# Kernel optimization log

Hardware: AMD Instinct MI355X
Metric: run time of the kernel (lower is better)

## Reference

```python
import jax, jax.numpy as jnp
import numpy as np

SCALE = 1.0

def setup_inputs() -> dict:
    key = jax.random.key(0)
    ks = jax.random.split(key, 7)
    B, S, I, O, R = 4, 4096, 1024, 1024, 256
    return {
        "x": jax.random.normal(ks[0], (B, S, I), dtype=jnp.float32),
        "base_weight": jax.random.normal(ks[1], (3 * O, I), dtype=jnp.float32) * 0.02,
        "base_bias": jax.random.normal(ks[2], (3 * O,), dtype=jnp.float32) * 0.02,
        "vera_A": jax.random.normal(ks[3], (R, I), dtype=jnp.float32) * 0.02,
        "vera_B": jax.random.normal(ks[4], (O, R), dtype=jnp.float32) * 0.02,
        "vera_d": jax.random.normal(ks[5], (2, R), dtype=jnp.float32) * 0.1,
        "vera_b": jax.random.normal(ks[6], (2, O), dtype=jnp.float32) * 0.1,
    }

def reference(x, base_weight, base_bias, vera_A, vera_B, vera_d, vera_b):
    # delta[k] = scale * diag(vera_b[k]) @ B @ diag(vera_d[k]) @ A  for k in {K, V}
    # implemented as (b[:,None]*B) @ (d[:,None]*A), batched over k via einsum
    O, I = vera_B.shape[0], vera_A.shape[1]
    deltas = SCALE * jnp.einsum("ko,or,kr,ri->koi", vera_b, vera_B, vera_d, vera_A)
    delta = deltas.reshape(2 * O, I)  # (2*O, I) stacked K,V deltas
    # kv_only=True: Q rows get zero delta, then K,V deltas
    zeros = jnp.zeros((base_weight.shape[0] - 2 * O, I), dtype=base_weight.dtype)
    full_delta = jnp.concatenate([zeros, delta], axis=0)  # (3*O, I)
    weight = base_weight + full_delta
    # linear: x @ weight.T + bias -> (B, S, 3*O)
    return jnp.einsum("bsi,oi->bso", x, weight) + base_bias
```

## Files before the change

kernel.cpp:

```cpp
#include <hip/hip_runtime.h>
#include <hip/hip_bf16.h>
#include <cstdint>
#include <cstddef>

typedef __bf16 bf16_t;
typedef __bf16 bf16x8 __attribute__((ext_vector_type(8)));
typedef __bf16 bf16x4 __attribute__((ext_vector_type(4)));
typedef float  f32x4  __attribute__((ext_vector_type(4)));
typedef float  f32x16 __attribute__((ext_vector_type(16)));

#define M_DIM 16384
#define N_DIM 3072
#define K_DIM 1024
#define R_DIM 256
#define O_DIM 1024

#define BM 256
#define BN 256
#define BK 64
#define NTILE (N_DIM / BN)
#define GRID_GEMM ((M_DIM / BM) * NTILE)
#define CHUNK_XCD (GRID_GEMM / 8)
#define SMEM_BYTES 131072

#define REGN(c, isB, kh) ((c) * 32768 + (isB) * 16384 + (kh) * 8192)

__device__ __forceinline__ void gload_lds16(const bf16_t* g, bf16_t* l) {
  __builtin_amdgcn_global_load_lds(
      (__attribute__((address_space(1))) void*)(g),
      (__attribute__((address_space(3))) void*)(l), 16, 0, 0);
}

__global__ __launch_bounds__(256) void prep_all(
    const float* __restrict__ x,
    const float* __restrict__ base_w,
    const float* __restrict__ vA,
    const float* __restrict__ vB,
    const float* __restrict__ vd,
    const float* __restrict__ vb,
    bf16_t* __restrict__ Wf,
    bf16_t* __restrict__ xh)
{
  const int blk = blockIdx.x;
  const int t = threadIdx.x;

  if (blk >= 384) {
    const size_t base = ((size_t)(blk - 384) * 256 + t) * 8;
    const f32x4 v0 = *(const f32x4*)(x + base);
    const f32x4 v1 = *(const f32x4*)(x + base + 4);
    bf16x8 o;
    o[0] = (bf16_t)v0[0]; o[1] = (bf16_t)v0[1]; o[2] = (bf16_t)v0[2]; o[3] = (bf16_t)v0[3];
    o[4] = (bf16_t)v1[0]; o[5] = (bf16_t)v1[1]; o[6] = (bf16_t)v1[2]; o[7] = (bf16_t)v1[3];
    *(bf16x8*)(xh + base) = o;
    return;
  }

  if (blk < 128) {
    const float* src = base_w + (size_t)blk * 8 * K_DIM;
    bf16_t*      dst = Wf + (size_t)blk * 8 * K_DIM;
#pragma unroll
    for (int rr = 0; rr < 8; ++rr) {
      const f32x4 v = *(const f32x4*)(src + rr * K_DIM + t * 4);
      bf16x4 ov;
      ov[0] = (bf16_t)v[0]; ov[1] = (bf16_t)v[1];
      ov[2] = (bf16_t)v[2]; ov[3] = (bf16_t)v[3];
      *(bf16x4*)(dst + rr * K_DIM + t * 4) = ov;
    }
    return;
  }

  const int rb = (blk - 128) * 8;
  const int k  = rb >> 10;
  const int ob = rb & 1023;

  __shared__ float coeffT[R_DIM][8];
  {
    const int r = t;
    const float d = vd[k * R_DIM + r];
#pragma unroll
    for (int rr = 0; rr < 8; ++rr) {
      const int o = ob + rr;
      coeffT[r][rr] = vb[k * O_DIM + o] * vB[(size_t)o * R_DIM + r] * d;
    }
  }
  __syncthreads();

  float acc[8][4];
#pragma unroll
  for (int rr = 0; rr < 8; ++rr)
#pragma unroll
    for (int c = 0; c < 4; ++c) acc[rr][c] = 0.0f;

  for (int r = 0; r < R_DIM; ++r) {
    const f32x4 av = *(const f32x4*)(vA + (size_t)r * K_DIM + t * 4);
    const f32x4 c0 = *(const f32x4*)&coeffT[r][0];
    const f32x4 c1 = *(const f32x4*)&coeffT[r][4];
#pragma unroll
    for (int rr = 0; rr < 8; ++rr) {
      const float cc = (rr < 4) ? c0[rr] : c1[rr - 4];
      acc[rr][0] += cc * av[0];
      acc[rr][1] += cc * av[1];
      acc[rr][2] += cc * av[2];
      acc[rr][3] += cc * av[3];
    }
  }

#pragma unroll
  for (int rr = 0; rr < 8; ++rr) {
    const size_t row = (size_t)(1024 + rb + rr);
    const f32x4 bw = *(const f32x4*)(base_w + row * K_DIM + t * 4);
    bf16x4 ov;
    ov[0] = (bf16_t)(bw[0] + acc[rr][0]);
    ov[1] = (bf16_t)(bw[1] + acc[rr][1]);
    ov[2] = (bf16_t)(bw[2] + acc[rr][2]);
    ov[3] = (bf16_t)(bw[3] + acc[rr][3]);
    *(bf16x4*)(Wf + row * K_DIM + t * 4) = ov;
  }
}

__global__ __launch_bounds__(512, 2) void gemm_qkv(
    const bf16_t* __restrict__ Xh,
    const bf16_t* __restrict__ W,
    const float*  __restrict__ bias,
    float* __restrict__ out)
{
  extern __shared__ __align__(16) bf16_t sm[];

  const int rawbid = blockIdx.x;
  const int bid = (rawbid & 7) * CHUNK_XCD + (rawbid >> 3);
  const int mt = bid / NTILE, nt = bid % NTILE;
  const int m0 = mt * BM, n0 = nt * BN;

  const int t = threadIdx.x;
  const int lane = t & 63;
  const int w = t >> 6;
  const int wm = w >> 2;
  const int wn = w & 3;

  const int srow = t >> 2;
  const int sig  = (t & 3) ^ ((t >> 3) & 3);
  const bf16_t* pA0 = Xh + (size_t)(m0 + srow) * K_DIM + sig * 8;
  const bf16_t* pA1 = pA0 + (size_t)128 * K_DIM;
  const bf16_t* pB0 = W  + (size_t)(n0 + srow) * K_DIM + sig * 8;
  const bf16_t* pB1 = pB0 + (size_t)128 * K_DIM;

  const int l31 = lane & 31;
  const int hi  = lane >> 5;
  const int swz = (l31 >> 1) & 3;
  const int sA  = (wm * 128 + l31) * 32;
  const int sB  = (wn * 64  + l31) * 32;
  const int sl0 = ((0 + hi) ^ swz) * 8;
  const int sl1 = ((2 + hi) ^ swz) * 8;

  f32x16 acc[4][2];
#pragma unroll
  for (int i = 0; i < 4; ++i)
#pragma unroll
    for (int j = 0; j < 2; ++j) acc[i][j] = (f32x16)0.0f;

#define STAGE(isB, c, kh, kb)                                              \
  do {                                                                     \
    const bf16_t* g0 = ((isB) ? pB0 : pA0) + (kb) + (kh) * 32;             \
    const bf16_t* g1 = ((isB) ? pB1 : pA1) + (kb) + (kh) * 32;             \
    bf16_t* l = sm + REGN(c, isB, kh) + w * 512;                           \
    gload_lds16(g0, l);                                                    \
    gload_lds16(g1, l + 4096);                                             \
  } while (0)

#define LOADA4(c, kh, ks)                                                  \
  {                                                                        \
    const bf16_t* base_ = sm + REGN(c, 0, kh) + sA + ((ks) ? sl1 : sl0);   \
    _Pragma("unroll") for (int i = 0; i < 4; ++i)                          \
        a[i] = *(const bf16x8*)(base_ + i * 1024);                         \
  }

#define LOADB2(c, kh, ks)                                                  \
  {                                                                        \
    const bf16_t* base_ = sm + REGN(c, 1, kh) + sB + ((ks) ? sl1 : sl0);   \
    b[0] = *(const bf16x8*)(base_);                                        \
    b[1] = *(const bf16x8*)(base_ + 1024);                                 \
  }

#define MFMA8()                                                            \
  __builtin_amdgcn_s_setprio(1);                                           \
  _Pragma("unroll") for (int i = 0; i < 4; ++i)                            \
    _Pragma("unroll") for (int j = 0; j < 2; ++j)                          \
      acc[i][j] = __builtin_amdgcn_mfma_f32_32x32x16_bf16(                 \
          a[i], b[j], acc[i][j], 0, 0, 0);                                 \
  __builtin_amdgcn_s_setprio(0);

#define WAITV(n) asm volatile("s_waitcnt vmcnt(" #n ")" ::: "memory")
#define BARRIER()                                                          \
  __builtin_amdgcn_s_barrier();                                            \
  asm volatile("" ::: "memory")

  bf16x8 a[4], b[2];

  STAGE(0, 0, 0, 0);
  STAGE(1, 0, 0, 0);
  STAGE(0, 0, 1, 0);
  STAGE(1, 0, 1, 0);
  WAITV(4);
  BARRIER();

  for (int tt = 0; tt < 15; ++tt) {
    const int c = tt & 1, cn = c ^ 1;
    const int kb = (tt + 1) * BK;

    LOADA4(c, 0, 0);
    LOADB2(c, 0, 0);
    STAGE(0, cn, 0, kb);
    BARRIER();
    MFMA8();

    LOADA4(c, 0, 1);
    LOADB2(c, 0, 1);
    STAGE(1, cn, 0, kb);
    WAITV(4);
    BARRIER();
    MFMA8();

    LOADA4(c, 1, 0);
    LOADB2(c, 1, 0);
    STAGE(0, cn, 1, kb);
    BARRIER();
    MFMA8();

    LOADA4(c, 1, 1);
    LOADB2(c, 1, 1);
    STAGE(1, cn, 1, kb);
    WAITV(4);
    BARRIER();
    MFMA8();
  }

  LOADA4(1, 0, 0);
  LOADB2(1, 0, 0);
  BARRIER();
  MFMA8();

  LOADA4(1, 0, 1);
  LOADB2(1, 0, 1);
  WAITV(0);
  BARRIER();
  MFMA8();

  LOADA4(1, 1, 0);
  LOADB2(1, 1, 0);
  BARRIER();
  MFMA8();

  LOADA4(1, 1, 1);
  LOADB2(1, 1, 1);
  BARRIER();
  MFMA8();

  const int hi4 = hi * 4;
#pragma unroll
  for (int j = 0; j < 2; ++j) {
    const int n = n0 + wn * 64 + j * 32 + l31;
    const float bv = bias[n];
#pragma unroll
    for (int i = 0; i < 4; ++i) {
      const size_t mb = (size_t)(m0 + wm * 128 + i * 32 + hi4);
#pragma unroll
      for (int r = 0; r < 16; ++r) {
        const size_t row = mb + (r & 3) + 8 * (r >> 2);
        out[row * N_DIM + n] = acc[i][j][r] + bv;
      }
    }
  }
#undef STAGE
#undef LOADA4
#undef LOADB2
#undef MFMA8
#undef WAITV
#undef BARRIER
}

#define FBM 128
#define FBN 128
#define FBK 32
template <bool PRECONV>
__global__ __launch_bounds__(256) void gemm128(
    const bf16_t* __restrict__ Xh,
    const float*  __restrict__ Xf,
    const bf16_t* __restrict__ W,
    const float*  __restrict__ bias,
    float* __restrict__ out)
{
  __shared__ bf16_t As[FBM * FBK];
  __shared__ bf16_t Bs[FBN * FBK];

  const int rawbid = blockIdx.x;
  const int nblk = (M_DIM / FBM) * (N_DIM / FBN);
  const int bid = (rawbid & 7) * (nblk / 8) + (rawbid >> 3);
  const int nt = bid % (N_DIM / FBN);
  const int mt = bid / (N_DIM / FBN);
  const int m0 = mt * FBM;
  const int n0 = nt * FBN;

  const int t = threadIdx.x;
  const int lane = t & 63;
  const int w = t >> 6;
  const int wm = w >> 1;
  const int wn = w & 1;

  const int r0 = t >> 2;
  const int c0 = (t & 3) * 8;

  const bf16_t* gB0 = W + (size_t)(n0 + r0) * K_DIM + c0;
  const bf16_t* gB1 = gB0 + (size_t)64 * K_DIM;
  bf16_t* lA0 = As + r0 * FBK + c0;
  bf16_t* lA1 = As + (r0 + 64) * FBK + c0;
  bf16_t* lB0 = Bs + r0 * FBK + c0;
  bf16_t* lB1 = Bs + (r0 + 64) * FBK + c0;

  const bf16_t* gA0h = nullptr; const bf16_t* gA1h = nullptr;
  const float*  gA0f = nullptr; const float*  gA1f = nullptr;
  if constexpr (PRECONV) {
    gA0h = Xh + (size_t)(m0 + r0) * K_DIM + c0;
    gA1h = gA0h + (size_t)64 * K_DIM;
  } else {
    gA0f = Xf + (size_t)(m0 + r0) * K_DIM + c0;
    gA1f = gA0f + (size_t)64 * K_DIM;
  }

  f32x4 acc[4][4];
#pragma unroll
  for (int i = 0; i < 4; ++i)
#pragma unroll
    for (int j = 0; j < 4; ++j) acc[i][j] = (f32x4){0.f, 0.f, 0.f, 0.f};

  const int row_a = wm * 64 + (lane & 15);
  const int row_b = wn * 64 + (lane & 15);
  const int kb = (lane >> 4) * 8;

  for (int k0 = 0; k0 < K_DIM; k0 += FBK) {
    if constexpr (PRECONV) {
      gload_lds16(gA0h + k0, lA0);
      gload_lds16(gA1h + k0, lA1);
    } else {
      const f32x4 u0 = *(const f32x4*)(gA0f + k0);
      const f32x4 u1 = *(const f32x4*)(gA0f + k0 + 4);
      const f32x4 u2 = *(const f32x4*)(gA1f + k0);
      const f32x4 u3 = *(const f32x4*)(gA1f + k0 + 4);
      bf16x8 a0, a1;
#pragma unroll
      for (int c = 0; c < 4; ++c) {
        a0[c] = (bf16_t)u0[c]; a0[c + 4] = (bf16_t)u1[c];
        a1[c] = (bf16_t)u2[c]; a1[c + 4] = (bf16_t)u3[c];
      }
      *(bf16x8*)lA0 = a0;
      *(bf16x8*)lA1 = a1;
    }
    gload_lds16(gB0 + k0, lB0);
    gload_lds16(gB1 + k0, lB1);
    __syncthreads();

    bf16x8 a[4], b[4];
#pragma unroll
    for (int i = 0; i < 4; ++i)
      a[i] = *(const bf16x8*)(As + (row_a + i * 16) * FBK + kb);
#pragma unroll
    for (int j = 0; j < 4; ++j)
      b[j] = *(const bf16x8*)(Bs + (row_b + j * 16) * FBK + kb);

#pragma unroll
    for (int i = 0; i < 4; ++i)
#pragma unroll
      for (int j = 0; j < 4; ++j)
        acc[i][j] = __builtin_amdgcn_mfma_f32_16x16x32_bf16(a[i], b[j], acc[i][j], 0, 0, 0);

    __syncthreads();
  }

  const int colg = lane & 15;
  const int rq = (lane >> 4) * 4;
#pragma unroll
  for (int j = 0; j < 4; ++j) {
    const int n = n0 + wn * 64 + j * 16 + colg;
    const float bv = bias[n];
#pragma unroll
    for (int i = 0; i < 4; ++i) {
      const size_t mb = (size_t)(m0 + wm * 64 + i * 16 + rq);
#pragma unroll
      for (int r = 0; r < 4; ++r)
        out[(mb + r) * N_DIM + n] = acc[i][j][r] + bv;
    }
  }
}

extern "C" void kernel_launch(void* const* d_in, const int* in_sizes, int n_in,
                              void* d_out, int out_size, void* d_ws, size_t ws_size,
                              hipStream_t stream) {
  const float* x      = (const float*)d_in[0];
  const float* base_w = (const float*)d_in[1];
  const float* base_b = (const float*)d_in[2];
  const float* vA     = (const float*)d_in[3];
  const float* vB     = (const float*)d_in[4];
  const float* vd     = (const float*)d_in[5];
  const float* vb     = (const float*)d_in[6];
  float* out = (float*)d_out;

  const size_t xh_off   = 8u * 1024 * 1024;
  const size_t xh_bytes = (size_t)M_DIM * K_DIM * sizeof(bf16_t);

  bf16_t* Wf = (bf16_t*)d_ws;
  const bool preconv = ws_size >= xh_off + xh_bytes;
  bf16_t* Xh = preconv ? (bf16_t*)((char*)d_ws + xh_off) : nullptr;

  static int smem_ok = -1;
  if (smem_ok < 0) {
    hipError_t e = hipFuncSetAttribute(
        reinterpret_cast<const void*>(&gemm_qkv),
        hipFuncAttributeMaxDynamicSharedMemorySize, SMEM_BYTES);
    smem_ok = (e == hipSuccess) ? 1 : 0;
  }

  prep_all<<<preconv ? 8576 : 384, 256, 0, stream>>>(x, base_w, vA, vB, vd, vb, Wf, Xh);

  if (preconv && smem_ok == 1) {
    gemm_qkv<<<GRID_GEMM, 512, SMEM_BYTES, stream>>>(Xh, Wf, base_b, out);
  } else if (preconv) {
    gemm128<true><<<(M_DIM / FBM) * (N_DIM / FBN), 256, 0, stream>>>(
        Xh, nullptr, Wf, base_b, out);
  } else {
    gemm128<false><<<(M_DIM / FBM) * (N_DIM / FBN), 256, 0, stream>>>(
        nullptr, x, Wf, base_b, out);
  }
}
```

Baseline: 389.5 us.

## Fuse fp32-to-bf16 conversion of x into the GEMM A-tile loading

Removes the separate pass that converted x to bf16 in workspace, and instead has the main GEMM load fp32 x into registers, convert, and write bf16 to LDS. The A loads are issued one stage ahead and written after a vmcnt wait, while B stays on direct global-to-LDS loads. This eliminates a full read/write pass over the activation, at the cost of doubled A-side global reads across N tiles, extra registers, and extra LDS-wait synchronisation in the main loop.

```diff
diff --git a/kernel.cpp b/kernel.cpp
--- a/kernel.cpp
+++ b/kernel.cpp
@@ -31,29 +31,16 @@
       (__attribute__((address_space(3))) void*)(l), 16, 0, 0);
 }
 
-__global__ __launch_bounds__(256) void prep_all(
-    const float* __restrict__ x,
+__global__ __launch_bounds__(256) void prep_weight(
     const float* __restrict__ base_w,
     const float* __restrict__ vA,
     const float* __restrict__ vB,
     const float* __restrict__ vd,
     const float* __restrict__ vb,
-    bf16_t* __restrict__ Wf,
-    bf16_t* __restrict__ xh)
+    bf16_t* __restrict__ Wf)
 {
   const int blk = blockIdx.x;
   const int t = threadIdx.x;
-
-  if (blk >= 384) {
-    const size_t base = ((size_t)(blk - 384) * 256 + t) * 8;
-    const f32x4 v0 = *(const f32x4*)(x + base);
-    const f32x4 v1 = *(const f32x4*)(x + base + 4);
-    bf16x8 o;
-    o[0] = (bf16_t)v0[0]; o[1] = (bf16_t)v0[1]; o[2] = (bf16_t)v0[2]; o[3] = (bf16_t)v0[3];
-    o[4] = (bf16_t)v1[0]; o[5] = (bf16_t)v1[1]; o[6] = (bf16_t)v1[2]; o[7] = (bf16_t)v1[3];
-    *(bf16x8*)(xh + base) = o;
-    return;
-  }
 
   if (blk < 128) {
     const float* src = base_w + (size_t)blk * 8 * K_DIM;
@@ -119,7 +106,7 @@
 }
 
 __global__ __launch_bounds__(512, 2) void gemm_qkv(
-    const bf16_t* __restrict__ Xh,
+    const float*  __restrict__ X,
     const bf16_t* __restrict__ W,
     const float*  __restrict__ bias,
     float* __restrict__ out)
@@ -139,9 +126,8 @@
 
   const int srow = t >> 2;
   const int sig  = (t & 3) ^ ((t >> 3) & 3);
-  const bf16_t* pA0 = Xh + (size_t)(m0 + srow) * K_DIM + sig * 8;
-  const bf16_t* pA1 = pA0 + (size_t)128 * K_DIM;
-  const bf16_t* pB0 = W  + (size_t)(n0 + srow) * K_DIM + sig * 8;
+  const float*  pX0 = X + (size_t)(m0 + srow) * K_DIM + sig * 8;
+  const bf16_t* pB0 = W + (size_t)(n0 + srow) * K_DIM + sig * 8;
   const bf16_t* pB1 = pB0 + (size_t)128 * K_DIM;
 
   const int l31 = lane & 31;
@@ -158,14 +144,37 @@
 #pragma unroll
     for (int j = 0; j < 2; ++j) acc[i][j] = (f32x16)0.0f;
 
-#define STAGE(isB, c, kh, kb)                                              \
+  f32x4 af[4];
+
+#define BSTAGE(c, kh, kb)                                                  \
   do {                                                                     \
-    const bf16_t* g0 = ((isB) ? pB0 : pA0) + (kb) + (kh) * 32;             \
-    const bf16_t* g1 = ((isB) ? pB1 : pA1) + (kb) + (kh) * 32;             \
-    bf16_t* l = sm + REGN(c, isB, kh) + w * 512;                           \
+    const bf16_t* g0 = pB0 + (kb) + (kh) * 32;                             \
+    const bf16_t* g1 = pB1 + (kb) + (kh) * 32;                             \
+    bf16_t* l = sm + REGN(c, 1, kh) + 8 * t;                               \
     gload_lds16(g0, l);                                                    \
     gload_lds16(g1, l + 4096);                                             \
   } while (0)
+
+#define AISSUE(kh, kb)                                                     \
+  {                                                                        \
+    const float* g_ = pX0 + (kb) + (kh) * 32;                              \
+    af[0] = *(const f32x4*)(g_);                                           \
+    af[1] = *(const f32x4*)(g_ + 4);                                       \
+    af[2] = *(const f32x4*)(g_ + 128 * K_DIM);                             \
+    af[3] = *(const f32x4*)(g_ + 128 * K_DIM + 4);                         \
+  }
+
+#define AWRITE(c, kh)                                                      \
+  {                                                                        \
+    bf16x8 w0_, w1_;                                                       \
+    _Pragma("unroll") for (int e = 0; e < 4; ++e) {                        \
+      w0_[e] = (bf16_t)af[0][e]; w0_[e + 4] = (bf16_t)af[1][e];            \
+      w1_[e] = (bf16_t)af[2][e]; w1_[e + 4] = (bf16_t)af[3][e];            \
+    }                                                                      \
+    bf16_t* l_ = sm + REGN(c, 0, kh) + 8 * t;                              \
+    *(bf16x8*)l_ = w0_;                                                    \
+    *(bf16x8*)(l_ + 4096) = w1_;                                           \
+  }
 
 #define LOADA4(c, kh, ks)                                                  \
   {                                                                        \
@@ -190,17 +199,20 @@
   __builtin_amdgcn_s_setprio(0);
 
 #define WAITV(n) asm volatile("s_waitcnt vmcnt(" #n ")" ::: "memory")
+#define LGKM0()  asm volatile("s_waitcnt lgkmcnt(0)" ::: "memory")
 #define BARRIER()                                                          \
   __builtin_amdgcn_s_barrier();                                            \
   asm volatile("" ::: "memory")
 
   bf16x8 a[4], b[2];
 
-  STAGE(0, 0, 0, 0);
-  STAGE(1, 0, 0, 0);
-  STAGE(0, 0, 1, 0);
-  STAGE(1, 0, 1, 0);
-  WAITV(4);
+  AISSUE(0, 0);
+  BSTAGE(0, 0, 0);
+  BSTAGE(0, 1, 0);
+  WAITV(2);
+  AWRITE(0, 0);
+  AISSUE(1, 0);
+  LGKM0();
   BARRIER();
 
   for (int tt = 0; tt < 15; ++tt) {
@@ -209,27 +221,31 @@
 
     LOADA4(c, 0, 0);
     LOADB2(c, 0, 0);
-    STAGE(0, cn, 0, kb);
     BARRIER();
     MFMA8();
 
     LOADA4(c, 0, 1);
     LOADB2(c, 0, 1);
-    STAGE(1, cn, 0, kb);
-    WAITV(4);
+    BSTAGE(cn, 0, kb);
+    WAITV(2);
+    AWRITE(c, 1);
+    AISSUE(0, kb);
+    LGKM0();
     BARRIER();
     MFMA8();
 
     LOADA4(c, 1, 0);
     LOADB2(c, 1, 0);
-    STAGE(0, cn, 1, kb);
     BARRIER();
     MFMA8();
 
     LOADA4(c, 1, 1);
     LOADB2(c, 1, 1);
-    STAGE(1, cn, 1, kb);
-    WAITV(4);
+    BSTAGE(cn, 1, kb);
+    WAITV(2);
+    AWRITE(cn, 0);
+    AISSUE(1, kb);
+    LGKM0();
     BARRIER();
     MFMA8();
   }
@@ -242,6 +258,8 @@
   LOADA4(1, 0, 1);
   LOADB2(1, 0, 1);
   WAITV(0);
+  AWRITE(1, 1);
+  LGKM0();
   BARRIER();
   MFMA8();
 
@@ -270,20 +288,21 @@
       }
     }
   }
-#undef STAGE
+#undef BSTAGE
+#undef AISSUE
+#undef AWRITE
 #undef LOADA4
 #undef LOADB2
 #undef MFMA8
 #undef WAITV
+#undef LGKM0
 #undef BARRIER
 }
 
 #define FBM 128
 #define FBN 128
 #define FBK 32
-template <bool PRECONV>
 __global__ __launch_bounds__(256) void gemm128(
-    const bf16_t* __restrict__ Xh,
     const float*  __restrict__ Xf,
     const bf16_t* __restrict__ W,
     const float*  __restrict__ bias,
@@ -311,20 +330,10 @@
 
   const bf16_t* gB0 = W + (size_t)(n0 + r0) * K_DIM + c0;
   const bf16_t* gB1 = gB0 + (size_t)64 * K_DIM;
-  bf16_t* lA0 = As + r0 * FBK + c0;
-  bf16_t* lA1 = As + (r0 + 64) * FBK + c0;
   bf16_t* lB0 = Bs + r0 * FBK + c0;
   bf16_t* lB1 = Bs + (r0 + 64) * FBK + c0;
-
-  const bf16_t* gA0h = nullptr; const bf16_t* gA1h = nullptr;
-  const float*  gA0f = nullptr; const float*  gA1f = nullptr;
-  if constexpr (PRECONV) {
-    gA0h = Xh + (size_t)(m0 + r0) * K_DIM + c0;
-    gA1h = gA0h + (size_t)64 * K_DIM;
-  } else {
-    gA0f = Xf + (size_t)(m0 + r0) * K_DIM + c0;
-    gA1f = gA0f + (size_t)64 * K_DIM;
-  }
+  const float* gA0f = Xf + (size_t)(m0 + r0) * K_DIM + c0;
+  const float* gA1f = gA0f + (size_t)64 * K_DIM;
 
   f32x4 acc[4][4];
 #pragma unroll
@@ -337,23 +346,18 @@
   const int kb = (lane >> 4) * 8;
 
   for (int k0 = 0; k0 < K_DIM; k0 += FBK) {
-    if constexpr (PRECONV) {
-      gload_lds16(gA0h + k0, lA0);
-      gload_lds16(gA1h + k0, lA1);
-    } else {
-      const f32x4 u0 = *(const f32x4*)(gA0f + k0);
-      const f32x4 u1 = *(const f32x4*)(gA0f + k0 + 4);
-      const f32x4 u2 = *(const f32x4*)(gA1f + k0);
-      const f32x4 u3 = *(const f32x4*)(gA1f + k0 + 4);
-      bf16x8 a0, a1;
-#pragma unroll
-      for (int c = 0; c < 4; ++c) {
-        a0[c] = (bf16_t)u0[c]; a0[c + 4] = (bf16_t)u1[c];
-        a1[c] = (bf16_t)u2[c]; a1[c + 4] = (bf16_t)u3[c];
-      }
-      *(bf16x8*)lA0 = a0;
-      *(bf16x8*)lA1 = a1;
-    }
+    const f32x4 u0 = *(const f32x4*)(gA0f + k0);
+    const f32x4 u1 = *(const f32x4*)(gA0f + k0 + 4);
+    const f32x4 u2 = *(const f32x4*)(gA1f + k0);
+    const f32x4 u3 = *(const f32x4*)(gA1f + k0 + 4);
+    bf16x8 a0, a1;
+#pragma unroll
+    for (int c = 0; c < 4; ++c) {
+      a0[c] = (bf16_t)u0[c]; a0[c + 4] = (bf16_t)u1[c];
+      a1[c] = (bf16_t)u2[c]; a1[c + 4] = (bf16_t)u3[c];
+    }
+    *(bf16x8*)(As + r0 * FBK + c0) = a0;
+    *(bf16x8*)(As + (r0 + 64) * FBK + c0) = a1;
     gload_lds16(gB0 + k0, lB0);
     gload_lds16(gB1 + k0, lB1);
     __syncthreads();
@@ -403,12 +407,7 @@
   const float* vb     = (const float*)d_in[6];
   float* out = (float*)d_out;
 
-  const size_t xh_off   = 8u * 1024 * 1024;
-  const size_t xh_bytes = (size_t)M_DIM * K_DIM * sizeof(bf16_t);
-
   bf16_t* Wf = (bf16_t*)d_ws;
-  const bool preconv = ws_size >= xh_off + xh_bytes;
-  bf16_t* Xh = preconv ? (bf16_t*)((char*)d_ws + xh_off) : nullptr;
 
   static int smem_ok = -1;
   if (smem_ok < 0) {
@@ -418,15 +417,12 @@
     smem_ok = (e == hipSuccess) ? 1 : 0;
   }
 
-  prep_all<<<preconv ? 8576 : 384, 256, 0, stream>>>(x, base_w, vA, vB, vd, vb, Wf, Xh);
-
-  if (preconv && smem_ok == 1) {
-    gemm_qkv<<<GRID_GEMM, 512, SMEM_BYTES, stream>>>(Xh, Wf, base_b, out);
-  } else if (preconv) {
-    gemm128<true><<<(M_DIM / FBM) * (N_DIM / FBN), 256, 0, stream>>>(
-        Xh, nullptr, Wf, base_b, out);
+  prep_weight<<<384, 256, 0, stream>>>(base_w, vA, vB, vd, vb, Wf);
+
+  if (smem_ok == 1) {
+    gemm_qkv<<<GRID_GEMM, 512, SMEM_BYTES, stream>>>(x, Wf, base_b, out);
   } else {
-    gemm128<false><<<(M_DIM / FBM) * (N_DIM / FBN), 256, 0, stream>>>(
-        nullptr, x, Wf, base_b, out);
+    gemm128<<<(M_DIM / FBM) * (N_DIM / FBN), 256, 0, stream>>>(
+        x, Wf, base_b, out);
   }
 }
```

New measurement: 425.9 us. 9.3% more time.
